# Kernel tuning notes

Hardware: AMD Instinct MI355X
Metric: run time of the kernel (lower is better)

## Reference

```python
import jax, jax.numpy as jnp
import numpy as np
import math

NUM_HEADS = 32
HEAD_DIM = 128  # had_dim in the torch module
BATCH, SEQ = 4, 4096
HIDDEN = NUM_HEADS * HEAD_DIM  # 4096


def _sylvester_hadamard(n):
    # Unnormalized +/-1 Hadamard matrix (matches get_hadK output for power-of-2 n).
    H = np.array([[1.0]], dtype=np.float32)
    while H.shape[0] < n:
        H = np.block([[H, H], [H, -H]])
    return H


def setup_inputs() -> dict:
    key = jax.random.key(0)
    x = jax.random.normal(key, (BATCH, SEQ, HIDDEN), dtype=jnp.float32)
    had_K = jnp.asarray(_sylvester_hadamard(NUM_HEADS))
    return {"x": x, "had_K": had_K}


def reference(x, had_K):
    # Faithful to: had_K @ x.reshape(-1, hidden//had_dim, had_dim) / sqrt(hidden//had_dim)
    init_shape = x.shape
    num_heads = init_shape[-1] // HEAD_DIM
    xr = x.reshape(-1, num_heads, HEAD_DIM)  # (B*S, heads, head_dim)
    scale = 1.0 / math.sqrt(num_heads)
    y = jnp.einsum('hk,bkd->bhd', had_K, xr) * scale  # Hadamard mix across heads
    return y.reshape(init_shape)
```

## Files before the change

### kernel.cpp

```cpp
#include <hip/hip_runtime.h>


#define HEADS 32
#define HDIM 128
#define ROW_F4 (HDIM / 4)
#define TOKEN_F4 (HEADS * ROW_F4)
#define BLOCK 256
#define DGROUPS ROW_F4
#define TOK_PER_BLOCK (BLOCK / DGROUPS)

__global__ __launch_bounds__(BLOCK)
void hadamard_heads_kernel(const float4* __restrict__ x,
                           float4* __restrict__ y,
                           int ntokens) {
    const int tid   = blockIdx.x * BLOCK + threadIdx.x;
    const int token = tid / DGROUPS;
    const int dg    = tid % DGROUPS;
    if (token >= ntokens) return;

    const size_t base = (size_t)token * TOKEN_F4 + dg;
    const float4* xp = x + base;

    float4 v[HEADS];
#pragma unroll
    for (int k = 0; k < HEADS; ++k) {
        v[k] = xp[k * ROW_F4];
    }

#pragma unroll
    for (int s = 1; s < HEADS; s <<= 1) {
#pragma unroll
        for (int k = 0; k < HEADS; ++k) {
            if ((k & s) == 0) {
                float4 a = v[k];
                float4 b = v[k + s];
                v[k]     = make_float4(a.x + b.x, a.y + b.y, a.z + b.z, a.w + b.w);
                v[k + s] = make_float4(a.x - b.x, a.y - b.y, a.z - b.z, a.w - b.w);
            }
        }
    }

    const float scale = 0.17677669529663687f;
    float4* yp = y + base;
#pragma unroll
    for (int k = 0; k < HEADS; ++k) {
        float4 a = v[k];
        yp[k * ROW_F4] = make_float4(a.x * scale, a.y * scale, a.z * scale, a.w * scale);
    }
}

extern "C" void kernel_launch(void* const* d_in, const int* in_sizes, int n_in,
                              void* d_out, int out_size, void* d_ws, size_t ws_size,
                              hipStream_t stream) {
    const float* x = (const float*)d_in[0];
    float* y = (float*)d_out;

    const int ntokens = in_sizes[0] / (HEADS * HDIM);
    const int blocks = (ntokens + TOK_PER_BLOCK - 1) / TOK_PER_BLOCK;

    hadamard_heads_kernel<<<blocks, BLOCK, 0, stream>>>(
        (const float4*)x, (float4*)y, ntokens);
}
```

Measured before the change: 431.0 us.

## Split each token's head butterfly across two half-waves with shuffle exchange and nontemporal IO

Each token is now handled by a 64-lane wave instead of 32 threads. Each half-wave does a 16-point butterfly over half of the heads, and the final stage is finished with a cross-half __shfl_xor(32) exchange plus a sign flip. This halves the registers each thread holds, which should raise occupancy and memory-level parallelism for this bandwidth-bound kernel. Loads and stores also become nontemporal so the streamed data does not pollute the cache. In exchange it adds shuffle traffic and doubles the thread count.

```diff
diff --git a/kernel.cpp b/kernel.cpp
--- a/kernel.cpp
+++ b/kernel.cpp
@@ -1,51 +1,64 @@
 #include <hip/hip_runtime.h>
 
 
+typedef float f4 __attribute__((ext_vector_type(4)));
+
 #define HEADS 32
-#define HDIM 128
-#define ROW_F4 (HDIM / 4)
+#define ROW_F4 32
 #define TOKEN_F4 (HEADS * ROW_F4)
 #define BLOCK 256
-#define DGROUPS ROW_F4
-#define TOK_PER_BLOCK (BLOCK / DGROUPS)
+#define TOK_PER_BLOCK (BLOCK / 64)
 
 __global__ __launch_bounds__(BLOCK)
-void hadamard_heads_kernel(const float4* __restrict__ x,
-                           float4* __restrict__ y,
+void hadamard_heads_kernel(const f4* __restrict__ x,
+                           f4* __restrict__ y,
                            int ntokens) {
     const int tid   = blockIdx.x * BLOCK + threadIdx.x;
-    const int token = tid / DGROUPS;
-    const int dg    = tid % DGROUPS;
+    const int token = tid >> 6;
+    const int lane  = tid & 63;
+    const int a     = lane >> 5;
+    const int dg    = lane & 31;
     if (token >= ntokens) return;
 
-    const size_t base = (size_t)token * TOKEN_F4 + dg;
-    const float4* xp = x + base;
+    const size_t base = (size_t)token * TOKEN_F4 + (size_t)a * 16 * ROW_F4 + dg;
+    const f4* xp = x + base;
+    f4* yp = y + base;
 
-    float4 v[HEADS];
+    f4 v[16];
 #pragma unroll
-    for (int k = 0; k < HEADS; ++k) {
-        v[k] = xp[k * ROW_F4];
+    for (int j = 0; j < 16; ++j) {
+        v[j] = __builtin_nontemporal_load(&xp[j * ROW_F4]);
     }
 
 #pragma unroll
-    for (int s = 1; s < HEADS; s <<= 1) {
+    for (int s = 1; s < 16; s <<= 1) {
 #pragma unroll
-        for (int k = 0; k < HEADS; ++k) {
-            if ((k & s) == 0) {
-                float4 a = v[k];
-                float4 b = v[k + s];
-                v[k]     = make_float4(a.x + b.x, a.y + b.y, a.z + b.z, a.w + b.w);
-                v[k + s] = make_float4(a.x - b.x, a.y - b.y, a.z - b.z, a.w - b.w);
+        for (int j = 0; j < 16; ++j) {
+            if ((j & s) == 0) {
+                f4 p = v[j];
+                f4 q = v[j + s];
+                v[j]     = p + q;
+                v[j + s] = p - q;
             }
         }
     }
 
+    const float sgn = (a == 0) ? 1.0f : -1.0f;
+#pragma unroll
+    for (int j = 0; j < 16; ++j) {
+        f4 o;
+        o.x = __shfl_xor(v[j].x, 32);
+        o.y = __shfl_xor(v[j].y, 32);
+        o.z = __shfl_xor(v[j].z, 32);
+        o.w = __shfl_xor(v[j].w, 32);
+        v[j] = o + sgn * v[j];
+    }
+
     const float scale = 0.17677669529663687f;
-    float4* yp = y + base;
 #pragma unroll
-    for (int k = 0; k < HEADS; ++k) {
-        float4 a = v[k];
-        yp[k * ROW_F4] = make_float4(a.x * scale, a.y * scale, a.z * scale, a.w * scale);
+    for (int j = 0; j < 16; ++j) {
+        f4 r = v[j] * scale;
+        __builtin_nontemporal_store(r, &yp[j * ROW_F4]);
     }
 }
 
@@ -55,9 +68,9 @@
     const float* x = (const float*)d_in[0];
     float* y = (float*)d_out;
 
-    const int ntokens = in_sizes[0] / (HEADS * HDIM);
+    const int ntokens = in_sizes[0] / (HEADS * ROW_F4 * 4);
     const int blocks = (ntokens + TOK_PER_BLOCK - 1) / TOK_PER_BLOCK;
 
     hadamard_heads_kernel<<<blocks, BLOCK, 0, stream>>>(
-        (const float4*)x, (float4*)y, ntokens);
+        (const f4*)x, (f4*)y, ntokens);
 }
```

Measured after the change: 416.3 us. 1.04x faster.
